# Performance work log

Measured on AMD Instinct MI355X. Metric: run time of the kernel, lower is better.

## Reference

```python
import jax, jax.numpy as jnp
import numpy as np

def setup_inputs() -> dict:
    key = jax.random.key(0)
    x = jax.random.normal(key, (2, 16, 2048, 64), dtype=jnp.float32)
    return {"x": x}

def reference(x):
    # Unnormalized attention: scores = q k^T (no softmax, no scaling), out = scores v,
    # with q = k = v = x. Faithful to the two torch.einsum calls.
    scores = jnp.einsum('bhid,bhjd->bhij', x, x)   # [B,H,T,T]
    out = jnp.einsum('bhij,bhjd->bhid', scores, x)  # [B,H,T,D]
    return out
```

## Files before the change

kernel.cpp:

```cpp
#include <hip/hip_runtime.h>


#define TDIM 2048
#define DDIM 64
#define NHEADS 32
#define NCH 16

typedef float f4 __attribute__((ext_vector_type(4)));
typedef float f32x4 __attribute__((ext_vector_type(4)));
typedef short bf16x8 __attribute__((ext_vector_type(8)));
typedef short s4 __attribute__((ext_vector_type(4)));

__device__ __forceinline__ void async_copy16(const void* g, void* l) {
    __builtin_amdgcn_global_load_lds(
        (const __attribute__((address_space(1))) void*)g,
        (__attribute__((address_space(3))) void*)l, 16, 0, 0);
}

__device__ __forceinline__ short f2bf(float f) {
    unsigned u = __builtin_bit_cast(unsigned, f);
    unsigned r = (u + 0x7fffu + ((u >> 16) & 1u)) >> 16;
    return (short)r;
}
__device__ __forceinline__ float bf2f(short s) {
    return __builtin_bit_cast(float, ((unsigned)(unsigned short)s) << 16);
}

__device__ __forceinline__ const bf16x8* fragp(const short* base, int row,
                                               int rowlen, int kelem) {
    const char* p = (const char*)(base + row * rowlen);
    return (const bf16x8*)(p + ((kelem * 2) ^ ((row & 7) << 4)));
}

__global__ __launch_bounds__(256) void k1_gram(const float* __restrict__ x,
                                               short* __restrict__ part) {
    __shared__ __align__(16) short XT[64 * 128];

    const int b    = blockIdx.x;
    const int tid  = threadIdx.x;
    const int lane = tid & 63;
    const int w    = tid >> 6;
    const int head = b >> 4, ch = b & 15;

    const float* xh = x + ((size_t)head * TDIM + ch * 128) * DDIM;

    const int rg = tid >> 4, cg = tid & 15;
    const int r0 = rg * 8, c4 = cg * 4;

    f4 v[8];
#pragma unroll
    for (int k = 0; k < 8; ++k)
        v[k] = *reinterpret_cast<const f4*>(xh + (size_t)(r0 + k) * DDIM + c4);

#pragma unroll
    for (int j = 0; j < 4; ++j) {
        bf16x8 pk;
#pragma unroll
        for (int k = 0; k < 8; ++k) pk[k] = f2bf(v[k][j]);
        const int c = c4 + j;
        *(bf16x8*)((char*)XT + c * 256 + ((2 * r0) ^ ((c & 7) << 4))) = pk;
    }
    __syncthreads();

    const int li = lane & 15, g = lane >> 4;
    const int iq0 = (w >> 1) * 2, jq0 = (w & 1) * 2;

    f32x4 acc[2][2];
#pragma unroll
    for (int a = 0; a < 2; ++a)
#pragma unroll
        for (int q = 0; q < 2; ++q) acc[a][q] = (f32x4){0.f, 0.f, 0.f, 0.f};

#pragma unroll
    for (int k0 = 0; k0 < 128; k0 += 32) {
        bf16x8 af[2], bv[2];
        af[0] = *fragp(XT, (iq0 + 0) * 16 + li, 128, k0 + 8 * g);
        af[1] = *fragp(XT, (iq0 + 1) * 16 + li, 128, k0 + 8 * g);
        bv[0] = *fragp(XT, (jq0 + 0) * 16 + li, 128, k0 + 8 * g);
        bv[1] = *fragp(XT, (jq0 + 1) * 16 + li, 128, k0 + 8 * g);
#pragma unroll
        for (int a = 0; a < 2; ++a)
#pragma unroll
            for (int q = 0; q < 2; ++q)
                acc[a][q] = __builtin_amdgcn_mfma_f32_16x16x32_bf16(
                    af[a], bv[q], acc[a][q], 0, 0, 0);
    }

    short* pp = part + (size_t)b * 4096;
#pragma unroll
    for (int a = 0; a < 2; ++a)
#pragma unroll
        for (int d = 0; d < 2; ++d) {
            s4 pk;
#pragma unroll
            for (int q = 0; q < 4; ++q) pk[q] = f2bf(acc[a][d][q]);
            *(s4*)(pp + ((((w * 2 + a) * 2 + d) * 64 + lane) << 2)) = pk;
        }
}

__global__ __launch_bounds__(256) void k2a_reduce(const short* __restrict__ part,
                                                  short* __restrict__ gbf) {
    const int b    = blockIdx.x;
    const int tid  = threadIdx.x;
    const int head = b >> 2, quarter = b & 3;

    const int f = quarter * 256 + tid;
    const short* ph = part + (size_t)head * NCH * 4096 + (f << 2);

    float s[4] = {0.f, 0.f, 0.f, 0.f};
#pragma unroll
    for (int c = 0; c < NCH; ++c) {
        const s4 v = *reinterpret_cast<const s4*>(ph + (size_t)c * 4096);
#pragma unroll
        for (int q = 0; q < 4; ++q) s[q] += bf2f(v[q]);
    }

    const int lane = f & 63, wad = f >> 6;
    const int w = wad >> 2, a = (wad >> 1) & 1, d = wad & 1;
    const int g = lane >> 4, li = lane & 15;
    const int iq0 = (w >> 1) * 2, jq0 = (w & 1) * 2;
    const int j = (jq0 + d) * 16 + li;
    char* gb = (char*)gbf + (size_t)head * 8192;
#pragma unroll
    for (int q = 0; q < 4; ++q) {
        const int i = (iq0 + a) * 16 + g * 4 + q;
        *(short*)(gb + i * 128 + ((2 * j) ^ ((i & 7) << 4))) = f2bf(s[q]);
    }
}

__global__ __launch_bounds__(256) void k2b_xg(const float* __restrict__ x,
                                              float* __restrict__ out,
                                              const short* __restrict__ gbf) {
    __shared__ __align__(16) short Xb[4096];
    __shared__ __align__(16) short Gb[4096];

    const int b    = blockIdx.x;
    const int tid  = threadIdx.x;
    const int lane = tid & 63;
    const int w    = tid >> 6;
    const int head = b >> 5, ch = b & 31;

    {
        const short* gg = gbf + (size_t)head * 4096 + w * 1024 + lane * 8;
        short* lg = Gb + w * 1024;
#pragma unroll
        for (int it = 0; it < 2; ++it)
            async_copy16(gg + it * 512, lg + it * 512);
    }

    const float* xh = x + ((size_t)head * TDIM + ch * 64) * DDIM;
#pragma unroll
    for (int e = 0; e < 4; ++e) {
        const int i4 = e * 256 + tid;
        const int r  = i4 >> 4;
        const int c4 = (i4 & 15) << 2;
        const f4 v = *reinterpret_cast<const f4*>(xh + (size_t)i4 * 4);
        s4 pk;
        pk[0] = f2bf(v[0]); pk[1] = f2bf(v[1]);
        pk[2] = f2bf(v[2]); pk[3] = f2bf(v[3]);
        *(s4*)((char*)Xb + r * 128 + ((2 * c4) ^ ((r & 7) << 4))) = pk;
    }
    __syncthreads();

    const int li = lane & 15, g = lane >> 4;

    f32x4 acc[4];
#pragma unroll
    for (int d = 0; d < 4; ++d) acc[d] = (f32x4){0.f, 0.f, 0.f, 0.f};

#pragma unroll
    for (int k0 = 0; k0 < 64; k0 += 32) {
        bf16x8 af, bv[4];
        af = *fragp(Xb, w * 16 + li, 64, k0 + 8 * g);
#pragma unroll
        for (int d = 0; d < 4; ++d)
            bv[d] = *fragp(Gb, d * 16 + li, 64, k0 + 8 * g);
#pragma unroll
        for (int d = 0; d < 4; ++d)
            acc[d] = __builtin_amdgcn_mfma_f32_16x16x32_bf16(
                af, bv[d], acc[d], 0, 0, 0);
    }

    float* oh = out + ((size_t)head * TDIM + ch * 64) * DDIM;
#pragma unroll
    for (int d = 0; d < 4; ++d)
#pragma unroll
        for (int q = 0; q < 4; ++q)
            oh[(w * 16 + g * 4 + q) * 64 + d * 16 + li] = acc[d][q];
}

extern "C" void kernel_launch(void* const* d_in, const int* in_sizes, int n_in,
                              void* d_out, int out_size, void* d_ws, size_t ws_size,
                              hipStream_t stream) {
    const float* x = (const float*)d_in[0];
    float* out  = (float*)d_out;
    short* part = (short*)d_ws;
    short* gbf  = part + (size_t)512 * 4096;

    k1_gram<<<NHEADS * NCH, 256, 0, stream>>>(x, part);
    k2a_reduce<<<128, 256, 0, stream>>>(part, gbf);
    k2b_xg<<<NHEADS * 32, 256, 0, stream>>>(x, out, gbf);
}
```

Measured before the change: 18.98 us.

## Emit swizzled bf16 copy of x in gram kernel and async-load it in xg

The gram kernel now runs 512 threads per block, each handling 4 rows instead of 8, with one output tile per wave. It also writes a pre-swizzled bf16 image of x to workspace. The final X·G kernel then loads that image directly into LDS with async global-to-LDS copies, skipping the fp32 reads and bf16 conversion. This halves the bytes read in the last kernel and removes its conversion work, at the cost of an extra global write in the first kernel and a different occupancy profile.

```diff
diff --git a/kernel.cpp b/kernel.cpp
--- a/kernel.cpp
+++ b/kernel.cpp
@@ -32,8 +32,9 @@
     return (const bf16x8*)(p + ((kelem * 2) ^ ((row & 7) << 4)));
 }
 
-__global__ __launch_bounds__(256) void k1_gram(const float* __restrict__ x,
-                                               short* __restrict__ part) {
+__global__ __launch_bounds__(512) void k1_gram(const float* __restrict__ x,
+                                               short* __restrict__ part,
+                                               short* __restrict__ xbf) {
     __shared__ __align__(16) short XT[64 * 128];
 
     const int b    = blockIdx.x;
@@ -44,58 +45,70 @@
 
     const float* xh = x + ((size_t)head * TDIM + ch * 128) * DDIM;
 
-    const int rg = tid >> 4, cg = tid & 15;
-    const int r0 = rg * 8, c4 = cg * 4;
-
-    f4 v[8];
-#pragma unroll
-    for (int k = 0; k < 8; ++k)
+    const int rg = tid >> 4;
+    const int cg = tid & 15;
+    const int r0 = rg * 4, c4 = cg * 4;
+
+    f4 v[4];
+#pragma unroll
+    for (int k = 0; k < 4; ++k)
         v[k] = *reinterpret_cast<const f4*>(xh + (size_t)(r0 + k) * DDIM + c4);
 
+    short pk[4][4];
+#pragma unroll
+    for (int k = 0; k < 4; ++k)
+#pragma unroll
+        for (int j = 0; j < 4; ++j) pk[k][j] = f2bf(v[k][j]);
+
 #pragma unroll
     for (int j = 0; j < 4; ++j) {
-        bf16x8 pk;
-#pragma unroll
-        for (int k = 0; k < 8; ++k) pk[k] = f2bf(v[k][j]);
         const int c = c4 + j;
-        *(bf16x8*)((char*)XT + c * 256 + ((2 * r0) ^ ((c & 7) << 4))) = pk;
+        s4 t4;
+#pragma unroll
+        for (int k = 0; k < 4; ++k) t4[k] = pk[k][j];
+        *(s4*)((char*)XT + c * 256 + ((2 * r0) ^ ((c & 7) << 4))) = t4;
+    }
+
+    {
+        char* img = (char*)xbf + (size_t)head * 262144;
+#pragma unroll
+        for (int k = 0; k < 4; ++k) {
+            const int R = ch * 128 + r0 + k;
+            s4 t4;
+#pragma unroll
+            for (int j = 0; j < 4; ++j) t4[j] = pk[k][j];
+            *(s4*)(img + (size_t)R * 128 + ((2 * c4) ^ ((R & 7) << 4))) = t4;
+        }
     }
     __syncthreads();
 
     const int li = lane & 15, g = lane >> 4;
-    const int iq0 = (w >> 1) * 2, jq0 = (w & 1) * 2;
-
-    f32x4 acc[2][2];
-#pragma unroll
-    for (int a = 0; a < 2; ++a)
-#pragma unroll
-        for (int q = 0; q < 2; ++q) acc[a][q] = (f32x4){0.f, 0.f, 0.f, 0.f};
+    const int i_tile = w >> 1, j0 = (w & 1) * 2;
+
+    f32x4 acc[2];
+#pragma unroll
+    for (int d = 0; d < 2; ++d) acc[d] = (f32x4){0.f, 0.f, 0.f, 0.f};
 
 #pragma unroll
     for (int k0 = 0; k0 < 128; k0 += 32) {
-        bf16x8 af[2], bv[2];
-        af[0] = *fragp(XT, (iq0 + 0) * 16 + li, 128, k0 + 8 * g);
-        af[1] = *fragp(XT, (iq0 + 1) * 16 + li, 128, k0 + 8 * g);
-        bv[0] = *fragp(XT, (jq0 + 0) * 16 + li, 128, k0 + 8 * g);
-        bv[1] = *fragp(XT, (jq0 + 1) * 16 + li, 128, k0 + 8 * g);
-#pragma unroll
-        for (int a = 0; a < 2; ++a)
-#pragma unroll
-            for (int q = 0; q < 2; ++q)
-                acc[a][q] = __builtin_amdgcn_mfma_f32_16x16x32_bf16(
-                    af[a], bv[q], acc[a][q], 0, 0, 0);
+        bf16x8 af, bv[2];
+        af = *fragp(XT, i_tile * 16 + li, 128, k0 + 8 * g);
+        bv[0] = *fragp(XT, (j0 + 0) * 16 + li, 128, k0 + 8 * g);
+        bv[1] = *fragp(XT, (j0 + 1) * 16 + li, 128, k0 + 8 * g);
+#pragma unroll
+        for (int d = 0; d < 2; ++d)
+            acc[d] = __builtin_amdgcn_mfma_f32_16x16x32_bf16(
+                af, bv[d], acc[d], 0, 0, 0);
     }
 
     short* pp = part + (size_t)b * 4096;
 #pragma unroll
-    for (int a = 0; a < 2; ++a)
-#pragma unroll
-        for (int d = 0; d < 2; ++d) {
-            s4 pk;
-#pragma unroll
-            for (int q = 0; q < 4; ++q) pk[q] = f2bf(acc[a][d][q]);
-            *(s4*)(pp + ((((w * 2 + a) * 2 + d) * 64 + lane) << 2)) = pk;
-        }
+    for (int d = 0; d < 2; ++d) {
+        s4 o;
+#pragma unroll
+        for (int q = 0; q < 4; ++q) o[q] = f2bf(acc[d][q]);
+        *(s4*)(pp + (((w * 2 + d) * 64 + lane) << 2)) = o;
+    }
 }
 
 __global__ __launch_bounds__(256) void k2a_reduce(const short* __restrict__ part,
@@ -115,21 +128,21 @@
         for (int q = 0; q < 4; ++q) s[q] += bf2f(v[q]);
     }
 
-    const int lane = f & 63, wad = f >> 6;
-    const int w = wad >> 2, a = (wad >> 1) & 1, d = wad & 1;
+    const int lane = f & 63, wd = f >> 6;
+    const int w = wd >> 1, d = wd & 1;
     const int g = lane >> 4, li = lane & 15;
-    const int iq0 = (w >> 1) * 2, jq0 = (w & 1) * 2;
-    const int j = (jq0 + d) * 16 + li;
+    const int i_tile = w >> 1, j_tile = (w & 1) * 2 + d;
+    const int j = j_tile * 16 + li;
     char* gb = (char*)gbf + (size_t)head * 8192;
 #pragma unroll
     for (int q = 0; q < 4; ++q) {
-        const int i = (iq0 + a) * 16 + g * 4 + q;
+        const int i = i_tile * 16 + g * 4 + q;
         *(short*)(gb + i * 128 + ((2 * j) ^ ((i & 7) << 4))) = f2bf(s[q]);
     }
 }
 
-__global__ __launch_bounds__(256) void k2b_xg(const float* __restrict__ x,
-                                              float* __restrict__ out,
+__global__ __launch_bounds__(256) void k2b_xg(float* __restrict__ out,
+                                              const short* __restrict__ xbf,
                                               const short* __restrict__ gbf) {
     __shared__ __align__(16) short Xb[4096];
     __shared__ __align__(16) short Gb[4096];
@@ -141,24 +154,14 @@
     const int head = b >> 5, ch = b & 31;
 
     {
+        const short* gx = xbf + (size_t)head * 131072 + ch * 4096 +
+                          w * 1024 + lane * 8;
         const short* gg = gbf + (size_t)head * 4096 + w * 1024 + lane * 8;
-        short* lg = Gb + w * 1024;
-#pragma unroll
-        for (int it = 0; it < 2; ++it)
-            async_copy16(gg + it * 512, lg + it * 512);
-    }
-
-    const float* xh = x + ((size_t)head * TDIM + ch * 64) * DDIM;
-#pragma unroll
-    for (int e = 0; e < 4; ++e) {
-        const int i4 = e * 256 + tid;
-        const int r  = i4 >> 4;
-        const int c4 = (i4 & 15) << 2;
-        const f4 v = *reinterpret_cast<const f4*>(xh + (size_t)i4 * 4);
-        s4 pk;
-        pk[0] = f2bf(v[0]); pk[1] = f2bf(v[1]);
-        pk[2] = f2bf(v[2]); pk[3] = f2bf(v[3]);
-        *(s4*)((char*)Xb + r * 128 + ((2 * c4) ^ ((r & 7) << 4))) = pk;
+#pragma unroll
+        for (int it = 0; it < 2; ++it) {
+            async_copy16(gx + it * 512, Xb + w * 1024 + it * 512);
+            async_copy16(gg + it * 512, Gb + w * 1024 + it * 512);
+        }
     }
     __syncthreads();
 
@@ -196,8 +199,9 @@
     float* out  = (float*)d_out;
     short* part = (short*)d_ws;
     short* gbf  = part + (size_t)512 * 4096;
-
-    k1_gram<<<NHEADS * NCH, 256, 0, stream>>>(x, part);
+    short* xbf  = gbf + (size_t)NHEADS * 4096;
+
+    k1_gram<<<NHEADS * NCH, 512, 0, stream>>>(x, part, xbf);
     k2a_reduce<<<128, 256, 0, stream>>>(part, gbf);
-    k2b_xg<<<NHEADS * 32, 256, 0, stream>>>(x, out, gbf);
-}
+    k2b_xg<<<NHEADS * 32, 256, 0, stream>>>(out, xbf, gbf);
+}
```

Result: slower. 22.63 us (+19.2%).
